# Kernel tuning notes

Measured on AMD Instinct MI355X. Metric: run time of the kernel, lower is better.

## Reference

```python
import jax, jax.numpy as jnp
import numpy as np

NUM_NEIGHBORS = 9  # cfg['num_neighbors']


def _cdist(a, b):
    """Euclidean cdist. a: [..., M, D], b: [..., N, D] -> [..., M, N]."""
    a2 = jnp.sum(a * a, axis=-1)[..., :, None]
    b2 = jnp.sum(b * b, axis=-1)[..., None, :]
    ab = jnp.einsum('...md,...nd->...mn', a, b)
    return jnp.sqrt(jnp.maximum(a2 + b2 - 2.0 * ab, 0.0))


def setup_inputs() -> dict:
    key = jax.random.key(0)
    k1, k2 = jax.random.split(key)
    B, P, D, N = 8, 784, 384, 16384
    embedding = jax.random.normal(k1, (B * P, D), dtype=jnp.float32)
    embedding_coreset = jax.random.normal(k2, (N, D), dtype=jnp.float32)
    return {"embedding": embedding, "embedding_coreset": embedding_coreset, "batch_size": B}


def reference(embedding, embedding_coreset, batch_size):
    D = embedding.shape[-1]
    # 1-NN of every patch against the coreset
    dists = _cdist(embedding, embedding_coreset)          # [B*P, N]
    patch_scores = jnp.min(dists, axis=1).reshape(batch_size, -1)   # [B, P]
    locations = jnp.argmin(dists, axis=1).reshape(batch_size, -1)   # [B, P]

    b = jnp.arange(batch_size)
    max_patches = jnp.argmax(patch_scores, axis=1)        # [B]
    emb = embedding.reshape(batch_size, -1, D)            # [B, P, D]
    max_feats = emb[b, max_patches]                       # [B, D]
    score = patch_scores[b, max_patches]                  # [B]
    nn_index = locations[b, max_patches]                  # [B]
    nn_sample = embedding_coreset[nn_index]               # [B, D]

    # k-NN of the nearest coreset sample within the coreset (support set)
    d_nn = _cdist(nn_sample, embedding_coreset)           # [B, N]
    _, support = jax.lax.top_k(-d_nn, NUM_NEIGHBORS)      # smallest dists, ascending -> [B, K]
    support_feats = embedding_coreset[support]            # [B, K, D]

    # distances from max patch feature to the support samples
    d_sup = _cdist(max_feats[:, None, :], support_feats)[:, 0, :]  # [B, K]
    weights = (1.0 - jax.nn.softmax(d_sup, axis=1))[:, 0]          # [B]
    return weights * score
```

## Files before the change

kernel.cpp:

```cpp
#include <hip/hip_runtime.h>
#include <hip/hip_bf16.h>
#include <math.h>

#define M_TOTAL 6272
#define N_CS    16384
#define D_DIM   384
#define BATCH   8
#define P_PATCH 784
#define KNN     9

#define MTILES  (M_TOTAL / 128)
#define NTILES2 (N_CS / 256)
#define NBLK    (M_TOTAL / 4)
#define PBB     196

typedef _Float16 half8 __attribute__((ext_vector_type(8)));
typedef float    floatx4 __attribute__((ext_vector_type(4)));

__device__ __forceinline__ void async_copy16(const void* g, void* l) {
    __builtin_amdgcn_global_load_lds(
        (const __attribute__((address_space(1))) void*)g,
        (__attribute__((address_space(3))) void*)l, 16, 0, 0);
}

__device__ __forceinline__ unsigned long long shfl_xor_u64(unsigned long long v, int mk) {
    int lo = __shfl_xor((int)(unsigned)v, mk, 64);
    int hi = __shfl_xor((int)(unsigned)(v >> 32), mk, 64);
    return ((unsigned long long)(unsigned)hi << 32) | (unsigned)lo;
}

__global__ void convert_all_kernel(const float* __restrict__ emb,
                                   const float* __restrict__ cs,
                                   _Float16* __restrict__ embh,
                                   _Float16* __restrict__ csh,
                                   float* __restrict__ cnorm) {
    int w = threadIdx.x >> 6, lane = threadIdx.x & 63;
    int row = blockIdx.x * 4 + w;
    if (row >= N_CS + M_TOTAL) return;
    bool is_cs = row < N_CS;
    const float* r = (is_cs ? cs + (size_t)row * D_DIM
                            : emb + (size_t)(row - N_CS) * D_DIM) + lane * 6;
    float2 a = *(const float2*)r;
    float2 b = *(const float2*)(r + 2);
    float2 c = *(const float2*)(r + 4);
    union { _Float16 h[2]; unsigned u; } p0, p1, p2;
    p0.h[0] = (_Float16)a.x; p0.h[1] = (_Float16)a.y;
    p1.h[0] = (_Float16)b.x; p1.h[1] = (_Float16)b.y;
    p2.h[0] = (_Float16)c.x; p2.h[1] = (_Float16)c.y;
    unsigned* dst = (unsigned*)(is_cs ? csh + (size_t)row * D_DIM
                                      : embh + (size_t)(row - N_CS) * D_DIM) + lane * 3;
    dst[0] = p0.u; dst[1] = p1.u; dst[2] = p2.u;
    if (is_cs) {
        float s = a.x * a.x + a.y * a.y + b.x * b.x + b.y * b.y + c.x * c.x + c.y * c.y;
#pragma unroll
        for (int mk = 1; mk <= 32; mk <<= 1) s += __shfl_xor(s, mk, 64);
        if (lane == 0) cnorm[row] = s;
    }
}

__global__ __launch_bounds__(256, 2) void mindist_mfma_kernel(
    const _Float16* __restrict__ embh, const _Float16* __restrict__ csh,
    const float* __restrict__ cnorm,
    float* __restrict__ pvals, int* __restrict__ pidx) {
    __shared__ _Float16 As[128 * 32];
    __shared__ _Float16 Bs[256 * 32];

    const int b    = blockIdx.x;
    const int bx   = b >> 6;
    const int by   = ((b & 7) << 3) | ((b >> 3) & 7);
    const int tid  = threadIdx.x;
    const int lane = tid & 63;
    const int w    = tid >> 6;
    const int wr   = w >> 1, wc = w & 1;
    const int row0  = bx * 128;
    const int cbase = by * 256;
    const int q   = lane >> 4;
    const int cl  = lane & 15;

    floatx4 acc[4][8];
#pragma unroll
    for (int mi = 0; mi < 4; ++mi)
#pragma unroll
        for (int nj = 0; nj < 8; ++nj) acc[mi][nj] = (floatx4){0.f, 0.f, 0.f, 0.f};

    float cn_l[8];
#pragma unroll
    for (int nj = 0; nj < 8; ++nj)
        cn_l[nj] = cnorm[cbase + wc * 128 + nj * 16 + cl];

    const int sub4 = lane >> 2;
    const int ch   = lane & 3;

    for (int kk = 0; kk < D_DIM; kk += 32) {
        __syncthreads();
#pragma unroll
        for (int i = 0; i < 6; ++i) {
            int inst = w * 6 + i;
            if (inst < 8) {
                int r  = inst * 16 + sub4;
                int sc = (ch ^ ((r >> 1) & 3)) * 8;
                async_copy16(embh + (size_t)(row0 + r) * D_DIM + kk + sc,
                             &As[inst * 512 + lane * 8]);
            } else {
                int blk = inst - 8;
                int r   = blk * 16 + sub4;
                int sc  = (ch ^ ((r >> 1) & 3)) * 8;
                async_copy16(csh + (size_t)(cbase + r) * D_DIM + kk + sc,
                             &Bs[blk * 512 + lane * 8]);
            }
        }
        __syncthreads();
        {
            half8 af[4], bf[8];
#pragma unroll
            for (int mi = 0; mi < 4; ++mi) {
                int R = wr * 64 + mi * 16 + cl;
                af[mi] = *(const half8*)&As[R * 32 + ((q ^ ((R >> 1) & 3)) * 8)];
            }
#pragma unroll
            for (int nj = 0; nj < 8; ++nj) {
                int R = wc * 128 + nj * 16 + cl;
                bf[nj] = *(const half8*)&Bs[R * 32 + ((q ^ ((R >> 1) & 3)) * 8)];
            }
#pragma unroll
            for (int mi = 0; mi < 4; ++mi)
#pragma unroll
                for (int nj = 0; nj < 8; ++nj)
                    acc[mi][nj] = __builtin_amdgcn_mfma_f32_16x16x32_f16(
                        af[mi], bf[nj], acc[mi][nj], 0, 0, 0);
        }
    }

    __syncthreads();
    float* smv = (float*)As;
    int*   smi = (int*)(As + 512);

#pragma unroll
    for (int mi = 0; mi < 4; ++mi) {
#pragma unroll
        for (int r = 0; r < 4; ++r) {
            float v = 3.4e38f; int idx = 0x7fffffff;
#pragma unroll
            for (int nj = 0; nj < 8; ++nj) {
                float d = cn_l[nj] - 2.f * acc[mi][nj][r];
                int   c = cbase + wc * 128 + nj * 16 + cl;
                if (d < v) { v = d; idx = c; }
            }
#pragma unroll
            for (int mk = 1; mk <= 8; mk <<= 1) {
                float v2 = __shfl_xor(v, mk, 64);
                int   i2 = __shfl_xor(idx, mk, 64);
                if (v2 < v || (v2 == v && i2 < idx)) { v = v2; idx = i2; }
            }
            if (cl == 0) {
                int rl = wr * 64 + mi * 16 + q * 4 + r;
                smv[rl * 2 + wc] = v;
                smi[rl * 2 + wc] = idx;
            }
        }
    }
    __syncthreads();
    if (tid < 128) {
        float v = smv[tid * 2];      int i = smi[tid * 2];
        float v1 = smv[tid * 2 + 1]; int i1 = smi[tid * 2 + 1];
        if (v1 < v) { v = v1; i = i1; }
        pvals[(size_t)(row0 + tid) * NTILES2 + by] = v;
        pidx[(size_t)(row0 + tid) * NTILES2 + by]  = i;
    }
}

__global__ void reduce_rescore_kernel(const float* __restrict__ pvals,
                                      const int* __restrict__ pidx,
                                      const float* __restrict__ emb,
                                      const float* __restrict__ cs,
                                      int* __restrict__ loc,
                                      unsigned long long* __restrict__ partial) {
    __shared__ unsigned long long keys[4];
    int w = threadIdx.x >> 6, lane = threadIdx.x & 63;
    int m = blockIdx.x * 4 + w;
    float v = pvals[(size_t)m * NTILES2 + lane];
    int   i = pidx[(size_t)m * NTILES2 + lane];
#pragma unroll
    for (int mk = 1; mk <= 32; mk <<= 1) {
        float v2 = __shfl_xor(v, mk, 64);
        int   i2 = __shfl_xor(i, mk, 64);
        if (v2 < v || (v2 == v && i2 < i)) { v = v2; i = i2; }
    }
    const float* a = emb + (size_t)m * D_DIM;
    const float* bp = cs + (size_t)i * D_DIM;
    float s = 0.f;
#pragma unroll
    for (int t = 0; t < D_DIM / 64; ++t) {
        float d = a[lane + t * 64] - bp[lane + t * 64];
        s += d * d;
    }
#pragma unroll
    for (int mk = 1; mk <= 32; mk <<= 1) s += __shfl_xor(s, mk, 64);
    if (lane == 0) {
        float sc = sqrtf(s);
        loc[m] = i;
        int p = m % P_PATCH;
        keys[w] = ((unsigned long long)__float_as_uint(sc) << 32) |
                  (unsigned)(0x7fffffff - p);
    }
    __syncthreads();
    if (threadIdx.x == 0) {
        unsigned long long k = keys[0];
        if (keys[1] > k) k = keys[1];
        if (keys[2] > k) k = keys[2];
        if (keys[3] > k) k = keys[3];
        partial[blockIdx.x] = k;
    }
}

__global__ void dnn_kernel(const float* __restrict__ cs,
                           const float* __restrict__ cnorm,
                           const unsigned long long* __restrict__ partial,
                           const int* __restrict__ loc,
                           float* __restrict__ dmat) {
    __shared__ int bnnS[BATCH];
    {
        int bb = threadIdx.x >> 5, l32 = threadIdx.x & 31;
        unsigned long long best = 0ull;
        for (int j = l32; j < PBB; j += 32) {
            unsigned long long k = partial[bb * PBB + j];
            if (k > best) best = k;
        }
#pragma unroll
        for (int mk = 1; mk <= 16; mk <<= 1) {
            unsigned long long o = shfl_xor_u64(best, mk);
            if (o > best) best = o;
        }
        if (l32 == 0) {
            int p = 0x7fffffff - (unsigned)(best & 0xffffffffull);
            bnnS[bb] = loc[bb * P_PATCH + p];
        }
    }
    __syncthreads();

    int lane = threadIdx.x & 63;
    int gw = (blockIdx.x * 256 + threadIdx.x) >> 6;
    float qv[BATCH][6];
#pragma unroll
    for (int b = 0; b < BATCH; ++b) {
        const float* qr = cs + (size_t)bnnS[b] * D_DIM + lane * 6;
#pragma unroll
        for (int j = 0; j < 6; ++j) qv[b][j] = qr[j];
    }
    for (int n = gw; n < N_CS; n += 1024) {
        const float* r = cs + (size_t)n * D_DIM + lane * 6;
        float x[6];
#pragma unroll
        for (int j = 0; j < 6; ++j) x[j] = r[j];
        float s[BATCH];
#pragma unroll
        for (int b = 0; b < BATCH; ++b) {
            float t = 0.f;
#pragma unroll
            for (int j = 0; j < 6; ++j) t += x[j] * qv[b][j];
            s[b] = t;
        }
#pragma unroll
        for (int b = 0; b < BATCH; ++b)
#pragma unroll
            for (int mk = 1; mk <= 32; mk <<= 1) s[b] += __shfl_xor(s[b], mk, 64);
        if (lane < BATCH) {
            float sv = s[0];
#pragma unroll
            for (int b = 1; b < BATCH; ++b) sv = (lane == b) ? s[b] : sv;
            dmat[(size_t)lane * N_CS + n] = cnorm[n] - 2.f * sv;
        }
    }
}

__device__ inline void merge9(float* av, int* ai, const float* bv, const int* bi) {
    float mv[KNN]; int mi[KNN];
    int x = 0, y = 0;
#pragma unroll
    for (int k = 0; k < KNN; ++k) {
        bool ta = (av[x] < bv[y]) || (av[x] == bv[y] && ai[x] < bi[y]);
        if (ta) { mv[k] = av[x]; mi[k] = ai[x]; ++x; }
        else    { mv[k] = bv[y]; mi[k] = bi[y]; ++y; }
    }
#pragma unroll
    for (int k = 0; k < KNN; ++k) { av[k] = mv[k]; ai[k] = mi[k]; }
}

__global__ void top9_final_kernel(const float* __restrict__ dmat,
                                  const float* __restrict__ emb,
                                  const float* __restrict__ cs,
                                  const unsigned long long* __restrict__ partial,
                                  float* __restrict__ out) {
    int b = blockIdx.x;
    int tid = threadIdx.x;
    __shared__ float lv[512][KNN];
    __shared__ int   li[512][KNN];
    __shared__ float mf[D_DIM];
    __shared__ float dsup[KNN];
    __shared__ float bscoreS;
    __shared__ int   bpatchS;

    if (tid < 64) {
        unsigned long long best = 0ull;
        for (int j = tid; j < PBB; j += 64) {
            unsigned long long k = partial[b * PBB + j];
            if (k > best) best = k;
        }
#pragma unroll
        for (int mk = 1; mk <= 32; mk <<= 1) {
            unsigned long long o = shfl_xor_u64(best, mk);
            if (o > best) best = o;
        }
        if (tid == 0) {
            bpatchS = 0x7fffffff - (unsigned)(best & 0xffffffffull);
            bscoreS = __uint_as_float((unsigned)(best >> 32));
        }
    }
    __syncthreads();
    int mp = bpatchS;
    const float* frow = emb + (size_t)(b * P_PATCH + mp) * D_DIM;
    for (int i = tid; i < D_DIM; i += 512) mf[i] = frow[i];

    float tv[KNN]; int ti[KNN];
#pragma unroll
    for (int k = 0; k < KNN; ++k) { tv[k] = 3.4e38f; ti[k] = 0x7fffffff; }
    for (int n = tid; n < N_CS; n += 512) {
        float d = dmat[(size_t)b * N_CS + n];
        if (d < tv[KNN - 1] || (d == tv[KNN - 1] && n < ti[KNN - 1])) {
            tv[KNN - 1] = d; ti[KNN - 1] = n;
#pragma unroll
            for (int k = KNN - 1; k > 0; --k) {
                if (tv[k] < tv[k - 1] || (tv[k] == tv[k - 1] && ti[k] < ti[k - 1])) {
                    float fv = tv[k]; tv[k] = tv[k - 1]; tv[k - 1] = fv;
                    int   iv = ti[k]; ti[k] = ti[k - 1]; ti[k - 1] = iv;
                }
            }
        }
    }
#pragma unroll
    for (int k = 0; k < KNN; ++k) { lv[tid][k] = tv[k]; li[tid][k] = ti[k]; }
    __syncthreads();
    for (int off = 256; off > 0; off >>= 1) {
        if (tid < off) {
            float av[KNN]; int ai[KNN]; float bv2[KNN]; int bi2[KNN];
#pragma unroll
            for (int k = 0; k < KNN; ++k) {
                av[k]  = lv[tid][k];        ai[k]  = li[tid][k];
                bv2[k] = lv[tid + off][k];  bi2[k] = li[tid + off][k];
            }
            merge9(av, ai, bv2, bi2);
#pragma unroll
            for (int k = 0; k < KNN; ++k) { lv[tid][k] = av[k]; li[tid][k] = ai[k]; }
        }
        __syncthreads();
    }
    {
        int k      = tid >> 5;
        int lane32 = tid & 31;
        if (k < KNN) {
            int idx = li[0][k];
            const float* r = cs + (size_t)idx * D_DIM;
            float s = 0.f;
            for (int i = lane32; i < D_DIM; i += 32) {
                float df = mf[i] - r[i];
                s += df * df;
            }
#pragma unroll
            for (int mk = 1; mk <= 16; mk <<= 1) s += __shfl_xor(s, mk, 64);
            if (lane32 == 0) dsup[k] = sqrtf(fmaxf(s, 0.f));
        }
    }
    __syncthreads();
    if (tid == 0) {
        float mx = dsup[0];
        for (int k = 1; k < KNN; ++k) mx = fmaxf(mx, dsup[k]);
        float sum = 0.f, e0 = 0.f;
        for (int k = 0; k < KNN; ++k) {
            float e = expf(dsup[k] - mx);
            sum += e;
            if (k == 0) e0 = e;
        }
        out[b] = (1.f - e0 / sum) * bscoreS;
    }
}

extern "C" void kernel_launch(void* const* d_in, const int* in_sizes, int n_in,
                              void* d_out, int out_size, void* d_ws, size_t ws_size,
                              hipStream_t stream) {
    (void)in_sizes; (void)n_in; (void)out_size; (void)ws_size;
    const float* emb = (const float*)d_in[0];
    const float* cs  = (const float*)d_in[1];
    float* out = (float*)d_out;

    char* p = (char*)d_ws;
    float* cnorm  = (float*)p;  p += (size_t)N_CS * 4;
    float* pvals  = (float*)p;  p += (size_t)M_TOTAL * NTILES2 * 4;
    int*   pidx   = (int*)p;    p += (size_t)M_TOTAL * NTILES2 * 4;
    int*   loc    = (int*)p;    p += (size_t)M_TOTAL * 4;
    p = (char*)(((size_t)p + 7) & ~(size_t)7);
    unsigned long long* partial = (unsigned long long*)p; p += NBLK * 8;
    float* dmat   = (float*)p;  p += (size_t)BATCH * N_CS * 4;
    p = (char*)(((size_t)p + 15) & ~(size_t)15);
    _Float16* embh = (_Float16*)p; p += (size_t)M_TOTAL * D_DIM * 2;
    _Float16* csh  = (_Float16*)p; p += (size_t)N_CS * D_DIM * 2;

    {
        int rows = N_CS + M_TOTAL;
        convert_all_kernel<<<(rows + 3) / 4, 256, 0, stream>>>(emb, cs, embh, csh, cnorm);
    }
    mindist_mfma_kernel<<<MTILES * NTILES2, 256, 0, stream>>>(embh, csh, cnorm,
                                                              pvals, pidx);
    reduce_rescore_kernel<<<NBLK, 256, 0, stream>>>(pvals, pidx, emb, cs, loc, partial);
    dnn_kernel<<<256, 256, 0, stream>>>(cs, cnorm, partial, loc, dmat);
    top9_final_kernel<<<BATCH, 512, 0, stream>>>(dmat, emb, cs, partial, out);
}
```

Measured before the change: 295.4 us.

## Double-buffer LDS tiles in the MFMA min-distance GEMM loop

The main K-loop of the min-distance kernel now uses two LDS buffers for the A and B tiles. The asynchronous global-to-LDS copy of the next K-slice is issued before the MFMA compute on the current slice, so global memory latency can overlap with compute, and one barrier per step is removed. In exchange the kernel uses twice as much shared memory per block (about 48 KB), which could limit how many blocks fit on a CU. The loop is manually peeled into stage/compute macros.

Measured after the change: 284.8 us. 3.6% less time.

```diff
diff --git a/kernel.cpp b/kernel.cpp
--- a/kernel.cpp
+++ b/kernel.cpp
@@ -62,8 +62,10 @@
     const _Float16* __restrict__ embh, const _Float16* __restrict__ csh,
     const float* __restrict__ cnorm,
     float* __restrict__ pvals, int* __restrict__ pidx) {
-    __shared__ _Float16 As[128 * 32];
-    __shared__ _Float16 Bs[256 * 32];
+    __shared__ _Float16 As0[128 * 32];
+    __shared__ _Float16 As1[128 * 32];
+    __shared__ _Float16 Bs0[256 * 32];
+    __shared__ _Float16 Bs1[256 * 32];
 
     const int b    = blockIdx.x;
     const int bx   = b >> 6;
@@ -91,49 +93,70 @@
     const int sub4 = lane >> 2;
     const int ch   = lane & 3;
 
-    for (int kk = 0; kk < D_DIM; kk += 32) {
+#define STAGE(AS, BS, KK)                                                     \
+    {                                                                         \
+        _Pragma("unroll")                                                     \
+        for (int i = 0; i < 6; ++i) {                                         \
+            int inst = w * 6 + i;                                             \
+            if (inst < 8) {                                                   \
+                int r  = inst * 16 + sub4;                                    \
+                int sc = (ch ^ ((r >> 1) & 3)) * 8;                           \
+                async_copy16(embh + (size_t)(row0 + r) * D_DIM + (KK) + sc,   \
+                             &AS[inst * 512 + lane * 8]);                     \
+            } else {                                                          \
+                int blk = inst - 8;                                           \
+                int r   = blk * 16 + sub4;                                    \
+                int sc  = (ch ^ ((r >> 1) & 3)) * 8;                          \
+                async_copy16(csh + (size_t)(cbase + r) * D_DIM + (KK) + sc,   \
+                             &BS[blk * 512 + lane * 8]);                      \
+            }                                                                 \
+        }                                                                     \
+    }
+
+#define COMPUTE(AS, BS)                                                       \
+    {                                                                         \
+        half8 af[4], bf[8];                                                   \
+        _Pragma("unroll")                                                     \
+        for (int mi = 0; mi < 4; ++mi) {                                      \
+            int R = wr * 64 + mi * 16 + cl;                                   \
+            af[mi] = *(const half8*)&AS[R * 32 + ((q ^ ((R >> 1) & 3)) * 8)]; \
+        }                                                                     \
+        _Pragma("unroll")                                                     \
+        for (int nj = 0; nj < 8; ++nj) {                                      \
+            int R = wc * 128 + nj * 16 + cl;                                  \
+            bf[nj] = *(const half8*)&BS[R * 32 + ((q ^ ((R >> 1) & 3)) * 8)]; \
+        }                                                                     \
+        _Pragma("unroll")                                                     \
+        for (int mi = 0; mi < 4; ++mi)                                        \
+            _Pragma("unroll")                                                 \
+            for (int nj = 0; nj < 8; ++nj)                                    \
+                acc[mi][nj] = __builtin_amdgcn_mfma_f32_16x16x32_f16(         \
+                    af[mi], bf[nj], acc[mi][nj], 0, 0, 0);                    \
+    }
+
+    STAGE(As0, Bs0, 0);
+    int kk = 0;
+#pragma unroll 1
+    for (int jj = 0; jj < 5; ++jj) {
         __syncthreads();
-#pragma unroll
-        for (int i = 0; i < 6; ++i) {
-            int inst = w * 6 + i;
-            if (inst < 8) {
-                int r  = inst * 16 + sub4;
-                int sc = (ch ^ ((r >> 1) & 3)) * 8;
-                async_copy16(embh + (size_t)(row0 + r) * D_DIM + kk + sc,
-                             &As[inst * 512 + lane * 8]);
-            } else {
-                int blk = inst - 8;
-                int r   = blk * 16 + sub4;
-                int sc  = (ch ^ ((r >> 1) & 3)) * 8;
-                async_copy16(csh + (size_t)(cbase + r) * D_DIM + kk + sc,
-                             &Bs[blk * 512 + lane * 8]);
-            }
-        }
+        STAGE(As1, Bs1, kk + 32);
+        COMPUTE(As0, Bs0);
         __syncthreads();
-        {
-            half8 af[4], bf[8];
-#pragma unroll
-            for (int mi = 0; mi < 4; ++mi) {
-                int R = wr * 64 + mi * 16 + cl;
-                af[mi] = *(const half8*)&As[R * 32 + ((q ^ ((R >> 1) & 3)) * 8)];
-            }
-#pragma unroll
-            for (int nj = 0; nj < 8; ++nj) {
-                int R = wc * 128 + nj * 16 + cl;
-                bf[nj] = *(const half8*)&Bs[R * 32 + ((q ^ ((R >> 1) & 3)) * 8)];
-            }
-#pragma unroll
-            for (int mi = 0; mi < 4; ++mi)
-#pragma unroll
-                for (int nj = 0; nj < 8; ++nj)
-                    acc[mi][nj] = __builtin_amdgcn_mfma_f32_16x16x32_f16(
-                        af[mi], bf[nj], acc[mi][nj], 0, 0, 0);
-        }
-    }
-
-    __syncthreads();
-    float* smv = (float*)As;
-    int*   smi = (int*)(As + 512);
+        STAGE(As0, Bs0, kk + 64);
+        COMPUTE(As1, Bs1);
+        kk += 64;
+    }
+    __syncthreads();
+    STAGE(As1, Bs1, kk + 32);
+    COMPUTE(As0, Bs0);
+    __syncthreads();
+    COMPUTE(As1, Bs1);
+#undef STAGE
+#undef COMPUTE
+
+    __syncthreads();
+    float* smv = (float*)As0;
+    int*   smi = (int*)(As0 + 512);
 
 #pragma unroll
     for (int mi = 0; mi < 4; ++mi) {
```

## Load MFMA fragments directly from global memory with register double-buffering

Applied to the files above, without the earlier changes.

Removes the LDS staging of A and B tiles and the two block barriers per K step in the distance GEMM. Each wave now loads its half8 fragments straight from global memory into registers and alternates between two register fragment sets, so loads for the next K slice overlap the MFMAs of the current one. The cost is no reuse of tiles across waves through LDS: every wave refetches shared rows through L1/L2 with poorly coalesced 16-byte loads. It also raises register pressure under the 2-blocks-per-SM launch bound.

Result: slower. 390.5 us (+32.2%).

```diff
diff --git a/kernel.cpp b/kernel.cpp
--- a/kernel.cpp
+++ b/kernel.cpp
@@ -16,12 +16,6 @@
 
 typedef _Float16 half8 __attribute__((ext_vector_type(8)));
 typedef float    floatx4 __attribute__((ext_vector_type(4)));
-
-__device__ __forceinline__ void async_copy16(const void* g, void* l) {
-    __builtin_amdgcn_global_load_lds(
-        (const __attribute__((address_space(1))) void*)g,
-        (__attribute__((address_space(3))) void*)l, 16, 0, 0);
-}
 
 __device__ __forceinline__ unsigned long long shfl_xor_u64(unsigned long long v, int mk) {
     int lo = __shfl_xor((int)(unsigned)v, mk, 64);
@@ -62,8 +56,8 @@
     const _Float16* __restrict__ embh, const _Float16* __restrict__ csh,
     const float* __restrict__ cnorm,
     float* __restrict__ pvals, int* __restrict__ pidx) {
-    __shared__ _Float16 As[128 * 32];
-    __shared__ _Float16 Bs[256 * 32];
+    __shared__ float smv[256];
+    __shared__ int   smi[256];
 
     const int b    = blockIdx.x;
     const int bx   = b >> 6;
@@ -88,52 +82,47 @@
     for (int nj = 0; nj < 8; ++nj)
         cn_l[nj] = cnorm[cbase + wc * 128 + nj * 16 + cl];
 
-    const int sub4 = lane >> 2;
-    const int ch   = lane & 3;
-
-    for (int kk = 0; kk < D_DIM; kk += 32) {
-        __syncthreads();
-#pragma unroll
-        for (int i = 0; i < 6; ++i) {
-            int inst = w * 6 + i;
-            if (inst < 8) {
-                int r  = inst * 16 + sub4;
-                int sc = (ch ^ ((r >> 1) & 3)) * 8;
-                async_copy16(embh + (size_t)(row0 + r) * D_DIM + kk + sc,
-                             &As[inst * 512 + lane * 8]);
-            } else {
-                int blk = inst - 8;
-                int r   = blk * 16 + sub4;
-                int sc  = (ch ^ ((r >> 1) & 3)) * 8;
-                async_copy16(csh + (size_t)(cbase + r) * D_DIM + kk + sc,
-                             &Bs[blk * 512 + lane * 8]);
-            }
-        }
-        __syncthreads();
-        {
-            half8 af[4], bf[8];
-#pragma unroll
-            for (int mi = 0; mi < 4; ++mi) {
-                int R = wr * 64 + mi * 16 + cl;
-                af[mi] = *(const half8*)&As[R * 32 + ((q ^ ((R >> 1) & 3)) * 8)];
-            }
-#pragma unroll
-            for (int nj = 0; nj < 8; ++nj) {
-                int R = wc * 128 + nj * 16 + cl;
-                bf[nj] = *(const half8*)&Bs[R * 32 + ((q ^ ((R >> 1) & 3)) * 8)];
-            }
-#pragma unroll
-            for (int mi = 0; mi < 4; ++mi)
-#pragma unroll
-                for (int nj = 0; nj < 8; ++nj)
-                    acc[mi][nj] = __builtin_amdgcn_mfma_f32_16x16x32_f16(
-                        af[mi], bf[nj], acc[mi][nj], 0, 0, 0);
-        }
-    }
-
-    __syncthreads();
-    float* smv = (float*)As;
-    int*   smi = (int*)(As + 512);
+    const _Float16* pa[4];
+    const _Float16* pb[8];
+#pragma unroll
+    for (int mi = 0; mi < 4; ++mi)
+        pa[mi] = embh + (size_t)(row0 + wr * 64 + mi * 16 + cl) * D_DIM + q * 8;
+#pragma unroll
+    for (int nj = 0; nj < 8; ++nj)
+        pb[nj] = csh + (size_t)(cbase + wc * 128 + nj * 16 + cl) * D_DIM + q * 8;
+
+#define LOADF(AF, BF, KK)                                                     \
+    {                                                                         \
+        _Pragma("unroll")                                                     \
+        for (int mi = 0; mi < 4; ++mi) AF[mi] = *(const half8*)(pa[mi] + (KK)); \
+        _Pragma("unroll")                                                     \
+        for (int nj = 0; nj < 8; ++nj) BF[nj] = *(const half8*)(pb[nj] + (KK)); \
+    }
+#define MFMAF(AF, BF)                                                         \
+    {                                                                         \
+        _Pragma("unroll")                                                     \
+        for (int mi = 0; mi < 4; ++mi)                                        \
+            _Pragma("unroll")                                                 \
+            for (int nj = 0; nj < 8; ++nj)                                    \
+                acc[mi][nj] = __builtin_amdgcn_mfma_f32_16x16x32_f16(         \
+                    AF[mi], BF[nj], acc[mi][nj], 0, 0, 0);                    \
+    }
+
+    half8 a0[4], b0[8], a1[4], b1[8];
+    LOADF(a0, b0, 0);
+#pragma unroll 1
+    for (int jj = 0; jj < 5; ++jj) {
+        int kk = jj * 64;
+        LOADF(a1, b1, kk + 32);
+        MFMAF(a0, b0);
+        LOADF(a0, b0, kk + 64);
+        MFMAF(a1, b1);
+    }
+    LOADF(a1, b1, 352);
+    MFMAF(a0, b0);
+    MFMAF(a1, b1);
+#undef LOADF
+#undef MFMAF
 
 #pragma unroll
     for (int mi = 0; mi < 4; ++mi) {
```
